# Performance work log

Measured on AMD Instinct MI355X. Metric: run time of the kernel, lower is better.

The kernel has to match this reference:

```python
import jax, jax.numpy as jnp
import numpy as np

M, N, H, K1, K2, C, B = 100000, 14000, 256, 16, 32, 7, 64
EPS = 1e-8


def setup_inputs() -> dict:
    key = jax.random.key(0)
    ks = jax.random.split(key, 8)
    embeds = jax.random.normal(ks[0], (M, H), dtype=jnp.float32)
    idx = jax.random.randint(ks[1], (N,), 0, M, dtype=jnp.int32)
    neighbors = jax.random.randint(ks[2], (N, K1), 0, M, dtype=jnp.int32)
    neighbors_2hop = jax.random.randint(ks[3], (N, K2), 0, M, dtype=jnp.int32)
    labels = (jnp.arange(N, dtype=jnp.int32) % C)  # perfectly balanced, as averageemb requires
    # prompt params (downstreamprompt weights, xavier-uniform [1,H])
    lim = float(np.sqrt(6.0 / (1 + H)))
    w_self = jax.random.uniform(ks[4], (1, H), jnp.float32, -lim, lim)
    w_n = jax.random.uniform(ks[5], (1, H), jnp.float32, -lim, lim)
    w_n2 = jax.random.uniform(ks[6], (1, H), jnp.float32, -lim, lim)
    # metanet (PromptVector): bottleneck adapter H -> B -> H
    k7, k8 = jax.random.split(ks[7])
    W1 = jax.random.normal(k7, (H, B), jnp.float32) * (1.0 / np.sqrt(H))
    b1 = jnp.zeros((B,), jnp.float32)
    W2 = jax.random.normal(k8, (B, H), jnp.float32) * (1.0 / np.sqrt(B))
    b2 = jnp.zeros((H,), jnp.float32)
    return {"embeds": embeds, "w_self": w_self, "w_n": w_n, "w_n2": w_n2,
            "W1": W1, "b1": b1, "W2": W2, "b2": b2,
            "idx": idx, "neighbors": neighbors, "neighbors_2hop": neighbors_2hop,
            "labels": labels}


def _cos(a, b):
    # torch.cosine_similarity with eps=1e-8 (clamped norms)
    num = jnp.sum(a * b, axis=-1)
    na = jnp.maximum(jnp.sqrt(jnp.sum(a * a, axis=-1)), EPS)
    nb = jnp.maximum(jnp.sqrt(jnp.sum(b * b, axis=-1)), EPS)
    return num / (na * nb)


def reference(embeds, w_self, w_n, w_n2, W1, b1, W2, b2,
              idx, neighbors, neighbors_2hop, labels):
    center = embeds[idx]                         # [N,H]
    ce = w_self * center                         # selfprompt: [N,H]
    nb = jnp.nan_to_num(w_n * embeds[neighbors])              # [N,K1,H]
    nb2 = jnp.nan_to_num(w_n2 * embeds[neighbors_2hop])       # [N,K2,H]
    nb_all = jnp.concatenate([nb, nb2], axis=1)  # [N,K1+K2,H]
    sim = _cos(ce[:, None, :], nb_all)           # [N,K]
    w = jax.nn.softmax(sim, axis=-1)
    weighted_neighbors = jnp.einsum('nk,nkh->nh', w, nb_all)
    inputs = weighted_neighbors + ce             # (dropout = identity at eval)
    prompts = jax.nn.elu(inputs @ W1 + b1) @ W2 + b2  # metanet adapter
    rawret = prompts + ce                        # [N,H]
    # averageemb: per-class mean (labels balanced, N/C per class)
    per_class = N // C
    ave = jax.ops.segment_sum(rawret, labels, num_segments=C) / per_class  # [C,H]
    ret = jax.nn.softmax(_cos(rawret[:, None, :], ave[None, :, :]), axis=1)  # [N,C]
    return ret
```

## Files before the change

### kernel.cpp

```cpp
#include <hip/hip_runtime.h>
#include <hip/hip_bf16.h>
#include <math.h>

#define H 256
#define NR 14000
#define MR 100000
#define K1C 16
#define K2C 32
#define KT 48
#define CC 7
#define EPSF 1e-8f
#define GP 448
#define CH2 32

typedef __attribute__((ext_vector_type(8))) unsigned short ushort8_t;

__device__ __forceinline__ float rdlane(float v, int l) {
    return __int_as_float(__builtin_amdgcn_readlane(__float_as_int(v), l));
}

__device__ __forceinline__ float dot4(const float4 a, const float4 b) {
    return a.x * b.x + a.y * b.y + a.z * b.z + a.w * b.w;
}

__device__ __forceinline__ unsigned short f2bf(float x) {
    __hip_bfloat16 h = __float2bfloat16(x);
    return *(unsigned short*)&h;
}

__global__ __launch_bounds__(256) void kE(const float* __restrict__ src,
                                          unsigned short* __restrict__ dst) {
    const size_t base = ((size_t)blockIdx.x * 256 + threadIdx.x) * 8;
    const float4 a = *(const float4*)(src + base);
    const float4 b = *(const float4*)(src + base + 4);
    ushort8_t o;
    o[0] = f2bf(a.x); o[1] = f2bf(a.y); o[2] = f2bf(a.z); o[3] = f2bf(a.w);
    o[4] = f2bf(b.x); o[5] = f2bf(b.y); o[6] = f2bf(b.z); o[7] = f2bf(b.w);
    *(ushort8_t*)(dst + base) = o;
}

__global__ __launch_bounds__(256, 2) void kA4(
    const float* __restrict__ embeds, const unsigned short* __restrict__ ebf,
    const float* __restrict__ w_self, const float* __restrict__ w_n,
    const float* __restrict__ w_n2, const int* __restrict__ idx,
    const int* __restrict__ nbr1, const int* __restrict__ nbr2,
    float* __restrict__ inbuf, float* __restrict__ cebuf)
{
    const int tid = threadIdx.x;
    const int wv = tid >> 6, lane = tid & 63;
    const int n = blockIdx.x * 4 + wv;
    const int g = lane >> 4, l = lane & 15;
    const int hb = l * 16;

    const int cidx = idx[n];
    int ridx = 0;
    if (lane < K1C) ridx = nbr1[n * K1C + lane];
    else if (lane < KT) ridx = nbr2[n * K2C + (lane - K1C)];

    const float* crow = embeds + (size_t)cidx * H + hb;
    float4 cv4[4], wsv4[4], wnv4[4], wn2v4[4];
#pragma unroll
    for (int j = 0; j < 4; ++j) {
        cv4[j]   = *(const float4*)(crow + 4 * j);
        wsv4[j]  = *(const float4*)(w_self + hb + 4 * j);
        wnv4[j]  = *(const float4*)(w_n    + hb + 4 * j);
        wn2v4[j] = *(const float4*)(w_n2   + hb + 4 * j);
    }

    int rows[12];
#pragma unroll
    for (int kk = 0; kk < 12; ++kk) rows[kk] = __shfl(ridx, kk * 4 + g);
    ushort8_t pb[24];
#pragma unroll
    for (int kk = 0; kk < 12; ++kk) {
        const unsigned short* rp = ebf + (size_t)rows[kk] * H + hb;
        pb[2 * kk]     = *(const ushort8_t*)(rp);
        pb[2 * kk + 1] = *(const ushort8_t*)(rp + 8);
    }

    float ce[16], wn[16], wn2[16];
    float na2 = 0.f;
#pragma unroll
    for (int j = 0; j < 4; ++j) {
        wn[4*j+0] = wnv4[j].x;  wn[4*j+1] = wnv4[j].y;
        wn[4*j+2] = wnv4[j].z;  wn[4*j+3] = wnv4[j].w;
        wn2[4*j+0] = wn2v4[j].x; wn2[4*j+1] = wn2v4[j].y;
        wn2[4*j+2] = wn2v4[j].z; wn2[4*j+3] = wn2v4[j].w;
        ce[4*j+0] = wsv4[j].x * cv4[j].x; ce[4*j+1] = wsv4[j].y * cv4[j].y;
        ce[4*j+2] = wsv4[j].z * cv4[j].z; ce[4*j+3] = wsv4[j].w * cv4[j].w;
        na2 += ce[4*j+0]*ce[4*j+0] + ce[4*j+1]*ce[4*j+1]
             + ce[4*j+2]*ce[4*j+2] + ce[4*j+3]*ce[4*j+3];
    }
#pragma unroll
    for (int m = 1; m <= 8; m <<= 1) na2 += __shfl_xor(na2, m);
    const float na = fmaxf(sqrtf(na2), EPSF);

    float acc[16];
#pragma unroll
    for (int i = 0; i < 16; ++i) acc[i] = 0.f;
    float lsum = 0.f;

#pragma unroll
    for (int kk = 0; kk < 12; ++kk) {
        const ushort8_t e0 = pb[2 * kk];
        const ushort8_t e1 = pb[2 * kk + 1];
        float nb[16];
#pragma unroll
        for (int i = 0; i < 8; ++i) {
            nb[i]     = __uint_as_float((unsigned)e0[i] << 16);
            nb[8 + i] = __uint_as_float((unsigned)e1[i] << 16);
        }
        float num = 0.f, nn = 0.f;
#pragma unroll
        for (int i = 0; i < 16; ++i) {
            const float w = (kk < 4) ? wn[i] : wn2[i];
            nb[i] *= w;
            num += ce[i] * nb[i];
            nn  += nb[i] * nb[i];
        }
#pragma unroll
        for (int m = 1; m <= 8; m <<= 1) {
            num += __shfl_xor(num, m);
            nn  += __shfl_xor(nn, m);
        }
        const float nbn = fmaxf(sqrtf(nn), EPSF);
        const float e = __expf(num / (nbn * na) - 1.0f);
        lsum += e;
#pragma unroll
        for (int i = 0; i < 16; ++i) acc[i] += e * nb[i];
    }
#pragma unroll
    for (int m = 16; m <= 32; m <<= 1) {
        lsum += __shfl_xor(lsum, m);
#pragma unroll
        for (int i = 0; i < 16; ++i) acc[i] += __shfl_xor(acc[i], m);
    }
    const float rl = 1.0f / lsum;
    if (g == 0) {
        float* ip = inbuf + (size_t)n * H + hb;
        float* cp = cebuf + (size_t)n * H + hb;
#pragma unroll
        for (int i = 0; i < 16; ++i) {
            ip[i] = acc[i] * rl + ce[i];
            cp[i] = ce[i];
        }
    }
}

__global__ __launch_bounds__(256, 2) void kB5(
    float* __restrict__ io, const float* __restrict__ cebuf,
    const float* __restrict__ W1, const float* __restrict__ b1,
    const float* __restrict__ W2, const float* __restrict__ b2)
{
    const int tid = threadIdx.x;
    const int wv = tid >> 6, lane = tid & 63;
    const int r0 = (blockIdx.x * 4 + wv) * 4;

    float4 in4[4];
#pragma unroll
    for (int r = 0; r < 4; ++r)
        in4[r] = *(const float4*)(io + (size_t)(r0 + r) * H + 4 * lane);

    float hid[4];
    const float bb = b1[lane];
#pragma unroll
    for (int r = 0; r < 4; ++r) hid[r] = bb;

#pragma unroll 8
    for (int l2 = 0; l2 < 64; ++l2) {
#pragma unroll
        for (int j = 0; j < 4; ++j) {
            const int h = 4 * l2 + j;
            const float w1v = W1[h * 64 + lane];
#pragma unroll
            for (int r = 0; r < 4; ++r) {
                const float src = (j == 0) ? in4[r].x : (j == 1) ? in4[r].y
                                 : (j == 2) ? in4[r].z : in4[r].w;
                hid[r] = fmaf(rdlane(src, l2), w1v, hid[r]);
            }
        }
    }
#pragma unroll
    for (int r = 0; r < 4; ++r)
        hid[r] = hid[r] > 0.f ? hid[r] : (__expf(hid[r]) - 1.0f);

    float4 p4[4];
    const float4 b2v = *(const float4*)(b2 + 4 * lane);
#pragma unroll
    for (int r = 0; r < 4; ++r) p4[r] = b2v;
#pragma unroll 8
    for (int b = 0; b < 64; ++b) {
        const float4 w2v = *(const float4*)(W2 + b * H + 4 * lane);
#pragma unroll
        for (int r = 0; r < 4; ++r) {
            const float hv = rdlane(hid[r], b);
            p4[r].x = fmaf(hv, w2v.x, p4[r].x);
            p4[r].y = fmaf(hv, w2v.y, p4[r].y);
            p4[r].z = fmaf(hv, w2v.z, p4[r].z);
            p4[r].w = fmaf(hv, w2v.w, p4[r].w);
        }
    }
#pragma unroll
    for (int r = 0; r < 4; ++r) {
        const float4 cev = *(const float4*)(cebuf + (size_t)(r0 + r) * H + 4 * lane);
        float4 ov;
        ov.x = p4[r].x + cev.x; ov.y = p4[r].y + cev.y;
        ov.z = p4[r].z + cev.z; ov.w = p4[r].w + cev.w;
        *(float4*)(io + (size_t)(r0 + r) * H + 4 * lane) = ov;
    }
}

__global__ __launch_bounds__(256) void kC1(
    const float* __restrict__ rawret, const int* __restrict__ labels,
    float* __restrict__ partial)
{
    const int t = threadIdx.x, j = blockIdx.x;
    const int nlo = j * CH2;
    const int nhi = min(nlo + CH2, NR);
    float acc[CC];
#pragma unroll
    for (int c = 0; c < CC; ++c) acc[c] = 0.f;
    for (int n = nlo; n < nhi; n += 4) {
        int lab[4]; float v[4];
#pragma unroll
        for (int u = 0; u < 4; ++u) {
            lab[u] = labels[n + u];
            v[u] = rawret[(size_t)(n + u) * H + t];
        }
#pragma unroll
        for (int u = 0; u < 4; ++u)
#pragma unroll
            for (int c = 0; c < CC; ++c) acc[c] += (lab[u] == c) ? v[u] : 0.f;
    }
#pragma unroll
    for (int c = 0; c < CC; ++c) partial[(size_t)(j * CC + c) * H + t] = acc[c];
}

__global__ __launch_bounds__(256) void kC2(
    const float* __restrict__ partial, float* __restrict__ ave)
{
    const int b = blockIdx.x, c = b >> 3, s = b & 7;
    const int hloc = threadIdx.x & 31, jg = threadIdx.x >> 5;
    const int h = 32 * s + hloc;
    float sum = 0.f;
#pragma unroll 8
    for (int j = jg; j < GP; j += 8)
        sum += partial[(size_t)(j * CC + c) * H + h];
    __shared__ float red[256];
    red[threadIdx.x] = sum;
    __syncthreads();
    if (jg == 0) {
#pragma unroll
        for (int t = 1; t < 8; ++t) sum += red[t * 32 + hloc];
        ave[c * H + h] = sum * (1.0f / 2000.0f);
    }
}

__global__ __launch_bounds__(256) void kD2(
    const float* __restrict__ rawret, const float* __restrict__ ave,
    float* __restrict__ out)
{
    const int tid = threadIdx.x;
    const int wv = tid >> 6, lane = tid & 63;
    const int n = blockIdx.x * 4 + wv;
    const float4 r4 = *(const float4*)(rawret + (size_t)n * H + 4 * lane);
    float nr2 = dot4(r4, r4);
#pragma unroll
    for (int m = 1; m <= 32; m <<= 1) nr2 += __shfl_xor(nr2, m);
    const float rn = fmaxf(sqrtf(nr2), EPSF);

    float e[CC];
    float s = 0.f;
#pragma unroll
    for (int c = 0; c < CC; ++c) {
        const float4 a4 = *(const float4*)(ave + c * H + 4 * lane);
        float d = dot4(r4, a4);
        float an = dot4(a4, a4);
#pragma unroll
        for (int m = 1; m <= 32; m <<= 1) {
            d  += __shfl_xor(d, m);
            an += __shfl_xor(an, m);
        }
        const float anorm = fmaxf(sqrtf(an), EPSF);
        const float sim = d / (rn * anorm);
        e[c] = __expf(sim - 1.0f);
        s += e[c];
    }
    const float rs = 1.0f / s;
    if (lane < CC) {
        float v = e[0];
#pragma unroll
        for (int c = 1; c < CC; ++c) v = (lane == c) ? e[c] : v;
        out[(size_t)n * CC + lane] = v * rs;
    }
}

extern "C" void kernel_launch(void* const* d_in, const int* in_sizes, int n_in,
                              void* d_out, int out_size, void* d_ws, size_t ws_size,
                              hipStream_t stream) {
    const float* embeds = (const float*)d_in[0];
    const float* w_self = (const float*)d_in[1];
    const float* w_n    = (const float*)d_in[2];
    const float* w_n2   = (const float*)d_in[3];
    const float* W1     = (const float*)d_in[4];
    const float* b1     = (const float*)d_in[5];
    const float* W2     = (const float*)d_in[6];
    const float* b2     = (const float*)d_in[7];
    const int* idx      = (const int*)d_in[8];
    const int* nbr1     = (const int*)d_in[9];
    const int* nbr2     = (const int*)d_in[10];
    const int* labels   = (const int*)d_in[11];
    float* out = (float*)d_out;

    float* rawret  = (float*)d_ws;
    float* cebuf   = rawret + (size_t)NR * H;
    float* partial = cebuf + (size_t)NR * H;
    float* ave     = partial + (size_t)GP * CC * H;
    unsigned short* ebf = (unsigned short*)(ave + CC * H + 8);

    kE<<<(MR * H) / (256 * 8), 256, 0, stream>>>(embeds, ebf);
    kA4<<<NR / 4, 256, 0, stream>>>(embeds, ebf, w_self, w_n, w_n2,
                                    idx, nbr1, nbr2, rawret, cebuf);
    kB5<<<NR / 16, 256, 0, stream>>>(rawret, cebuf, W1, b1, W2, b2);
    kC1<<<GP, 256, 0, stream>>>(rawret, labels, partial);
    kC2<<<56, 256, 0, stream>>>(partial, ave);
    kD2<<<NR / 4, 256, 0, stream>>>(rawret, ave, out);
}
```

Baseline: 310.0 us.

## Fuse per-class partial sums into adapter kernel and batch cosine reductions

The adapter kernel now also accumulates each block's rows into per-wave shared-memory class buckets and writes per-block class partials, so the separate class-sum pass that re-read rawret is removed. The partials buffer reuses the bf16 embedding scratch area, which is dead after the gather kernel. The final softmax kernel computes the class-mean norms once per block and reduces all seven dot products plus the row norm in one batched shuffle tree instead of fourteen separate ones. In exchange, the adapter kernel uses more shared memory and two extra barriers, and the reduce kernel now sums over 875 partials instead of 448.

```diff
diff --git a/kernel.cpp b/kernel.cpp
--- a/kernel.cpp
+++ b/kernel.cpp
@@ -10,8 +10,7 @@
 #define KT 48
 #define CC 7
 #define EPSF 1e-8f
-#define GP 448
-#define CH2 32
+#define NB 875
 
 typedef __attribute__((ext_vector_type(8))) unsigned short ushort8_t;
 
@@ -147,13 +146,20 @@
     }
 }
 
-__global__ __launch_bounds__(256, 2) void kB5(
+__global__ __launch_bounds__(256, 2) void kBC(
     float* __restrict__ io, const float* __restrict__ cebuf,
     const float* __restrict__ W1, const float* __restrict__ b1,
-    const float* __restrict__ W2, const float* __restrict__ b2)
+    const float* __restrict__ W2, const float* __restrict__ b2,
+    const int* __restrict__ labels, float* __restrict__ partial)
 {
+    __shared__ float rep[4 * CC * H];
     const int tid = threadIdx.x;
     const int wv = tid >> 6, lane = tid & 63;
+#pragma unroll
+    for (int i = 4 * tid; i < 4 * CC * H; i += 4 * 256)
+        *(float4*)(rep + i) = make_float4(0.f, 0.f, 0.f, 0.f);
+    __syncthreads();
+
     const int r0 = (blockIdx.x * 4 + wv) * 4;
 
     float4 in4[4];
@@ -207,33 +213,18 @@
         ov.x = p4[r].x + cev.x; ov.y = p4[r].y + cev.y;
         ov.z = p4[r].z + cev.z; ov.w = p4[r].w + cev.w;
         *(float4*)(io + (size_t)(r0 + r) * H + 4 * lane) = ov;
-    }
-}
-
-__global__ __launch_bounds__(256) void kC1(
-    const float* __restrict__ rawret, const int* __restrict__ labels,
-    float* __restrict__ partial)
-{
-    const int t = threadIdx.x, j = blockIdx.x;
-    const int nlo = j * CH2;
-    const int nhi = min(nlo + CH2, NR);
-    float acc[CC];
-#pragma unroll
-    for (int c = 0; c < CC; ++c) acc[c] = 0.f;
-    for (int n = nlo; n < nhi; n += 4) {
-        int lab[4]; float v[4];
-#pragma unroll
-        for (int u = 0; u < 4; ++u) {
-            lab[u] = labels[n + u];
-            v[u] = rawret[(size_t)(n + u) * H + t];
-        }
-#pragma unroll
-        for (int u = 0; u < 4; ++u)
-#pragma unroll
-            for (int c = 0; c < CC; ++c) acc[c] += (lab[u] == c) ? v[u] : 0.f;
-    }
-#pragma unroll
-    for (int c = 0; c < CC; ++c) partial[(size_t)(j * CC + c) * H + t] = acc[c];
+        const int lab = labels[r0 + r];
+        float* dst = rep + ((wv * CC + lab) * H) + 4 * lane;
+        float4 cur = *(float4*)dst;
+        cur.x += ov.x; cur.y += ov.y; cur.z += ov.z; cur.w += ov.w;
+        *(float4*)dst = cur;
+    }
+    __syncthreads();
+    for (int c = 0; c < CC; ++c) {
+        const float s = rep[(0 * CC + c) * H + tid] + rep[(1 * CC + c) * H + tid]
+                      + rep[(2 * CC + c) * H + tid] + rep[(3 * CC + c) * H + tid];
+        partial[((size_t)blockIdx.x * CC + c) * H + tid] = s;
+    }
 }
 
 __global__ __launch_bounds__(256) void kC2(
@@ -243,9 +234,9 @@
     const int hloc = threadIdx.x & 31, jg = threadIdx.x >> 5;
     const int h = 32 * s + hloc;
     float sum = 0.f;
-#pragma unroll 8
-    for (int j = jg; j < GP; j += 8)
-        sum += partial[(size_t)(j * CC + c) * H + h];
+#pragma unroll 5
+    for (int j = jg; j < NB; j += 8)
+        sum += partial[((size_t)j * CC + c) * H + h];
     __shared__ float red[256];
     red[threadIdx.x] = sum;
     __syncthreads();
@@ -256,34 +247,42 @@
     }
 }
 
-__global__ __launch_bounds__(256) void kD2(
+__global__ __launch_bounds__(256) void kD3(
     const float* __restrict__ rawret, const float* __restrict__ ave,
     float* __restrict__ out)
 {
+    __shared__ float lan[CC];
     const int tid = threadIdx.x;
     const int wv = tid >> 6, lane = tid & 63;
+    for (int c = wv; c < CC; c += 4) {
+        const float4 a4 = *(const float4*)(ave + c * H + 4 * lane);
+        float an = dot4(a4, a4);
+#pragma unroll
+        for (int m = 1; m <= 32; m <<= 1) an += __shfl_xor(an, m);
+        if (lane == 0) lan[c] = fmaxf(sqrtf(an), EPSF);
+    }
+    __syncthreads();
+
     const int n = blockIdx.x * 4 + wv;
     const float4 r4 = *(const float4*)(rawret + (size_t)n * H + 4 * lane);
-    float nr2 = dot4(r4, r4);
-#pragma unroll
-    for (int m = 1; m <= 32; m <<= 1) nr2 += __shfl_xor(nr2, m);
-    const float rn = fmaxf(sqrtf(nr2), EPSF);
-
+    float pd[8];
+#pragma unroll
+    for (int c = 0; c < CC; ++c) {
+        const float4 a4 = *(const float4*)(ave + c * H + 4 * lane);
+        pd[c] = dot4(r4, a4);
+    }
+    pd[7] = dot4(r4, r4);
+#pragma unroll
+    for (int m = 1; m <= 32; m <<= 1) {
+#pragma unroll
+        for (int i = 0; i < 8; ++i) pd[i] += __shfl_xor(pd[i], m);
+    }
+    const float rn = fmaxf(sqrtf(pd[7]), EPSF);
     float e[CC];
     float s = 0.f;
 #pragma unroll
     for (int c = 0; c < CC; ++c) {
-        const float4 a4 = *(const float4*)(ave + c * H + 4 * lane);
-        float d = dot4(r4, a4);
-        float an = dot4(a4, a4);
-#pragma unroll
-        for (int m = 1; m <= 32; m <<= 1) {
-            d  += __shfl_xor(d, m);
-            an += __shfl_xor(an, m);
-        }
-        const float anorm = fmaxf(sqrtf(an), EPSF);
-        const float sim = d / (rn * anorm);
-        e[c] = __expf(sim - 1.0f);
+        e[c] = __expf(pd[c] / (rn * lan[c]) - 1.0f);
         s += e[c];
     }
     const float rs = 1.0f / s;
@@ -314,15 +313,14 @@
 
     float* rawret  = (float*)d_ws;
     float* cebuf   = rawret + (size_t)NR * H;
-    float* partial = cebuf + (size_t)NR * H;
-    float* ave     = partial + (size_t)GP * CC * H;
+    float* ave     = cebuf + (size_t)NR * H;
     unsigned short* ebf = (unsigned short*)(ave + CC * H + 8);
+    float* partial = (float*)ebf;
 
     kE<<<(MR * H) / (256 * 8), 256, 0, stream>>>(embeds, ebf);
     kA4<<<NR / 4, 256, 0, stream>>>(embeds, ebf, w_self, w_n, w_n2,
                                     idx, nbr1, nbr2, rawret, cebuf);
-    kB5<<<NR / 16, 256, 0, stream>>>(rawret, cebuf, W1, b1, W2, b2);
-    kC1<<<GP, 256, 0, stream>>>(rawret, labels, partial);
+    kBC<<<NB, 256, 0, stream>>>(rawret, cebuf, W1, b1, W2, b2, labels, partial);
     kC2<<<56, 256, 0, stream>>>(partial, ave);
-    kD2<<<NR / 4, 256, 0, stream>>>(rawret, ave, out);
-}
+    kD3<<<NR / 4, 256, 0, stream>>>(rawret, ave, out);
+}
```

Result: slower. 329.5 us (+6.3%).
